# Performance work log

Measured on AMD Instinct MI355X. Metric: run time of the kernel, lower is better.

Reference implementation:

```python
import jax, jax.numpy as jnp
import numpy as np

AGENT_RADIUS = 0.3
B, F, H1, H21, H22, C, K = 262144, 5, 128, 32, 32, 2, 8


def _linear_init(k, fan_in, fan_out):
    lim = 1.0 / np.sqrt(fan_in)
    kw, kb = jax.random.split(k)
    W = jax.random.uniform(kw, (fan_out, fan_in), jnp.float32, -lim, lim)
    b = jax.random.uniform(kb, (fan_out,), jnp.float32, -lim, lim)
    return W, b


def setup_inputs() -> dict:
    key = jax.random.key(0)
    ks = jax.random.split(key, 9)
    W1, b1 = _linear_init(ks[0], F, H1)
    W21, b21 = _linear_init(ks[1], H1, H21)
    W22, b22 = _linear_init(ks[2], H1, H22)
    W31, b31 = _linear_init(ks[3], H21, C)
    W32, b32 = _linear_init(ks[4], H22, C)
    x = jax.random.normal(ks[5], (B, F), jnp.float32)
    mean = jax.random.normal(ks[6], (F,), jnp.float32) * 0.1
    std = jax.random.uniform(ks[7], (F,), jnp.float32, 0.5, 1.5)
    obs_xy = jax.random.uniform(ks[8], (K, 2), jnp.float32, -10.0, 10.0)
    obstacles = jnp.concatenate([obs_xy, jnp.full((K, 1), 0.5, jnp.float32)], axis=1)  # [K,3] = (ox,oy,r)
    return {"x": x, "mean": mean, "std": std,
            "W1": W1, "b1": b1, "W21": W21, "b21": b21, "W22": W22, "b22": b22,
            "W31": W31, "b31": b31, "W32": W32, "b32": b32,
            "obstacles": obstacles, "sgn": 1}


def _barriernet(x, mean, std, W1, b1, W21, b21, W22, b22, W31, b31, W32, b32, obstacles):
    nB = x.shape[0]
    x0 = x * std + mean
    h1 = jax.nn.relu(x @ W1.T + b1)                 # [B, H1]
    x21 = jax.nn.relu(h1 @ W21.T + b21)             # [B, H21]
    x22 = jax.nn.relu(h1 @ W22.T + b22)             # [B, H22]
    x31 = x21 @ W31.T + b31                          # [B, 2]  QP linear term p
    x32 = 4.0 * jax.nn.sigmoid(x22 @ W32.T + b32)    # [B, 2]  CBF class-K gains

    xo = x0 * std + mean  # module denormalizes twice inside dCBF (faithful to source)
    px, py, theta = xo[:, 0], xo[:, 1], xo[:, 2]
    oppx, oppy = xo[:, 3], xo[:, 4]
    cos_t, sin_t = jnp.cos(theta), jnp.sin(theta)

    # K static obstacles (broadcast) + 1 per-sample opponent -> nobs = K+1
    ox = jnp.concatenate([jnp.broadcast_to(obstacles[:, 0], (nB, K)), oppx[:, None]], axis=1)
    oy = jnp.concatenate([jnp.broadcast_to(obstacles[:, 1], (nB, K)), oppy[:, None]], axis=1)
    orr = jnp.concatenate([jnp.broadcast_to(obstacles[:, 2], (nB, K)),
                           jnp.full((nB, 1), AGENT_RADIUS, x.dtype)], axis=1)
    dx = px[:, None] - ox                            # [B, nobs]
    dy = py[:, None] - oy
    barrier = dx * dx + dy * dy - orr * orr          # [B, nobs]
    LgLf1 = 2.0 * dx * cos_t[:, None] + 2.0 * dy * sin_t[:, None]

    # QP: min 0.5 u^T I u + p^T u  s.t.  g1*u1 <= h  (second G column is 0)
    g1 = -LgLf1                                      # [B, nobs]
    hvec = (x32[:, 0] * x32[:, 1])[:, None] * barrier
    safe_g = jnp.where(g1 != 0.0, g1, 1.0)
    ratio = hvec / safe_g
    upper = jnp.min(jnp.where(g1 > 0.0, ratio, jnp.inf), axis=1)   # tightest u1 upper bound
    lower = jnp.max(jnp.where(g1 < 0.0, ratio, -jnp.inf), axis=1)  # tightest u1 lower bound
    u1 = jnp.clip(-x31[:, 0], lower, upper)          # exact KKT solution of the 1-D QP
    u2 = -x31[:, 1]                                  # unconstrained coordinate
    return jnp.stack([u1, u2], axis=1)               # [B, 2]


def reference(x, mean, std, W1, b1, W21, b21, W22, b22, W31, b31, W32, b32, obstacles, sgn):
    return _barriernet(x, mean, std, W1, b1, W21, b21, W22, b22, W31, b31, W32, b32, obstacles)
```

## Files before the change

### kernel.cpp

```cpp
#include <hip/hip_runtime.h>
#include <math.h>

typedef __attribute__((ext_vector_type(8))) short short8v;
typedef __attribute__((ext_vector_type(4))) float f32x4;

#define BLOCK 256
#define WPB   4
#define GRID  1024

__device__ inline unsigned int pk_bf16(float lo, float hi) {
    unsigned int r;
    asm("v_cvt_pk_bf16_f32 %0, %1, %2" : "=v"(r) : "v"(lo), "v"(hi));
    return r;
}
__device__ inline short8v as_s8(uint4 v) { union { uint4 u; short8v s; } c; c.u = v; return c.s; }

__global__ __launch_bounds__(BLOCK, 2) void bnet(
    const float* __restrict__ x,
    const float* __restrict__ meanp, const float* __restrict__ stdp,
    const float* __restrict__ W1,  const float* __restrict__ b1,
    const float* __restrict__ W21, const float* __restrict__ b21,
    const float* __restrict__ W22, const float* __restrict__ b22,
    const float* __restrict__ W31, const float* __restrict__ b31,
    const float* __restrict__ W32, const float* __restrict__ b32,
    const float* __restrict__ obstacles,
    float* __restrict__ out, int nB)
{
    __shared__ uint4 w1frag[8 * 64];
    __shared__ uint4 fragB[16 * 64];
    __shared__ float obl[32];

    const int t = threadIdx.x;

    {
        uint4 z = {0u, 0u, 0u, 0u};
        w1frag[t] = z; w1frag[t + 256] = z;
    }
    __syncthreads();
    if (t < 128) {
        int m = t & 15, g = t >> 4;
        int u = 16 * g + m;
        const float* wr = W1 + u * 5;
        uint4 v;
        v.x = pk_bf16(wr[0], wr[1]);
        v.y = pk_bf16(wr[2], wr[3]);
        v.z = pk_bf16(wr[4], b1[u]);
        v.w = 0u;
        w1frag[g * 64 + m] = v;
    }
    if (t < 8) {
        obl[t]      = obstacles[t * 3];
        obl[8 + t]  = obstacles[t * 3 + 1];
        float rr    = obstacles[t * 3 + 2];
        obl[16 + t] = rr * rr;
    }
    {
        const float4* w21v = (const float4*)W21;
        const float4* w22v = (const float4*)W22;
        #pragma unroll
        for (int e = 0; e < 4; ++e) {
            int g4   = t + e * 256;
            int uo   = g4 >> 5;
            int h0   = (g4 & 31) << 2;
            int ks   = h0 >> 5;
            int jh   = (h0 >> 4) & 1;
            int qq   = (h0 >> 2) & 3;
            int ln   = (qq << 4) | (uo & 15);
            int half = uo >> 4;
            float4 f1 = w21v[g4];
            float4 f2 = w22v[g4];
            unsigned int* dA = (unsigned int*)&fragB[(half * 4 + ks) * 64 + ln];
            unsigned int* dB = (unsigned int*)&fragB[(8 + half * 4 + ks) * 64 + ln];
            dA[jh * 2] = pk_bf16(f1.x, f1.y); dA[jh * 2 + 1] = pk_bf16(f1.z, f1.w);
            dB[jh * 2] = pk_bf16(f2.x, f2.y); dB[jh * 2 + 1] = pk_bf16(f2.z, f2.w);
        }
    }
    __syncthreads();

    const int lane = t & 63;
    const int q    = lane >> 4;
    const int r15  = lane & 15;
    const bool q0  = (q == 0);
    const int wid    = blockIdx.x * WPB + (t >> 6);
    const int nwaves = GRID * WPB;

    short8v bfr[16];
    #pragma unroll
    for (int i = 0; i < 16; ++i) bfr[i] = as_s8(fragB[i * 64 + lane]);

    float bi21[8], bi22[8];
    float c31_0[8], c31_1[8], c32_0[8], c32_1[8];
    {
        const int o = 4 * q;
        *(float4*)&bi21[0]  = *(const float4*)(b21 + o);
        *(float4*)&bi21[4]  = *(const float4*)(b21 + 16 + o);
        *(float4*)&bi22[0]  = *(const float4*)(b22 + o);
        *(float4*)&bi22[4]  = *(const float4*)(b22 + 16 + o);
        *(float4*)&c31_0[0] = *(const float4*)(W31 + o);
        *(float4*)&c31_0[4] = *(const float4*)(W31 + 16 + o);
        *(float4*)&c31_1[0] = *(const float4*)(W31 + 32 + o);
        *(float4*)&c31_1[4] = *(const float4*)(W31 + 48 + o);
        *(float4*)&c32_0[0] = *(const float4*)(W32 + o);
        *(float4*)&c32_0[4] = *(const float4*)(W32 + 16 + o);
        *(float4*)&c32_1[0] = *(const float4*)(W32 + 32 + o);
        *(float4*)&c32_1[4] = *(const float4*)(W32 + 48 + o);
    }
    const float b31_0 = b31[0], b31_1 = b31[1];
    const float b32_0 = b32[0], b32_1 = b32[1];

    float s2[5], ms[5];
    #pragma unroll
    for (int c = 0; c < 5; ++c) { float m = meanp[c], s = stdp[c]; s2[c] = s * s; ms[c] = fmaf(m, s, m); }

    const int ntiles = (nB + 15) >> 4;
    const int npairs = (ntiles + 1) >> 1;

    int pair = wid;
    if (pair >= npairs) return;

    float xrA[5], xrB[5];
    {
        int rA = pair * 32 + r15;      if (rA >= nB) rA = nB - 1;
        int rB = pair * 32 + 16 + r15; if (rB >= nB) rB = nB - 1;
        const float* pA = x + (size_t)rA * 5;
        const float* pB = x + (size_t)rB * 5;
        #pragma unroll
        for (int c = 0; c < 5; ++c) { xrA[c] = pA[c]; xrB[c] = pB[c]; }
    }

    while (true) {
        const int nxt = pair + nwaves;
        const bool has = nxt < npairs;
        float xA2[5], xB2[5];
        if (has) {
            int rA = nxt * 32 + r15;      if (rA >= nB) rA = nB - 1;
            int rB = nxt * 32 + 16 + r15; if (rB >= nB) rB = nB - 1;
            const float* pA = x + (size_t)rA * 5;
            const float* pB = x + (size_t)rB * 5;
            #pragma unroll
            for (int c = 0; c < 5; ++c) { xA2[c] = pA[c]; xB2[c] = pB[c]; }
        }
        const int baseA = pair * 32;

        short8v xfA, xfB;
        {
            float one = q0 ? 1.0f : 0.0f;
            uint4 va, vb;
            va.x = pk_bf16(q0 ? xrA[0] : 0.f, q0 ? xrA[1] : 0.f);
            va.y = pk_bf16(q0 ? xrA[2] : 0.f, q0 ? xrA[3] : 0.f);
            va.z = pk_bf16(q0 ? xrA[4] : 0.f, one);
            va.w = 0u;
            vb.x = pk_bf16(q0 ? xrB[0] : 0.f, q0 ? xrB[1] : 0.f);
            vb.y = pk_bf16(q0 ? xrB[2] : 0.f, q0 ? xrB[3] : 0.f);
            vb.z = pk_bf16(q0 ? xrB[4] : 0.f, one);
            vb.w = 0u;
            xfA = as_s8(va); xfB = as_s8(vb);
        }

        short8v afA[4], afB[4];
        #pragma unroll
        for (int ks = 0; ks < 4; ++ks) {
            f32x4 z = {0.f, 0.f, 0.f, 0.f};
            short8v w0 = as_s8(w1frag[(2 * ks) * 64 + lane]);
            short8v w1v = as_s8(w1frag[(2 * ks + 1) * 64 + lane]);
            f32x4 hA0 = __builtin_amdgcn_mfma_f32_16x16x32_bf16(w0,  xfA, z, 0, 0, 0);
            f32x4 hA1 = __builtin_amdgcn_mfma_f32_16x16x32_bf16(w1v, xfA, z, 0, 0, 0);
            f32x4 hB0 = __builtin_amdgcn_mfma_f32_16x16x32_bf16(w0,  xfB, z, 0, 0, 0);
            f32x4 hB1 = __builtin_amdgcn_mfma_f32_16x16x32_bf16(w1v, xfB, z, 0, 0, 0);
            uint4 va, vb;
            va.x = pk_bf16(fmaxf(hA0[0], 0.f), fmaxf(hA0[1], 0.f));
            va.y = pk_bf16(fmaxf(hA0[2], 0.f), fmaxf(hA0[3], 0.f));
            va.z = pk_bf16(fmaxf(hA1[0], 0.f), fmaxf(hA1[1], 0.f));
            va.w = pk_bf16(fmaxf(hA1[2], 0.f), fmaxf(hA1[3], 0.f));
            vb.x = pk_bf16(fmaxf(hB0[0], 0.f), fmaxf(hB0[1], 0.f));
            vb.y = pk_bf16(fmaxf(hB0[2], 0.f), fmaxf(hB0[3], 0.f));
            vb.z = pk_bf16(fmaxf(hB1[0], 0.f), fmaxf(hB1[1], 0.f));
            vb.w = pk_bf16(fmaxf(hB1[2], 0.f), fmaxf(hB1[3], 0.f));
            afA[ks] = as_s8(va); afB[ks] = as_s8(vb);
        }

        f32x4 a21aA = {bi21[0], bi21[1], bi21[2], bi21[3]};
        f32x4 a21bA = {bi21[4], bi21[5], bi21[6], bi21[7]};
        f32x4 a22aA = {bi22[0], bi22[1], bi22[2], bi22[3]};
        f32x4 a22bA = {bi22[4], bi22[5], bi22[6], bi22[7]};
        f32x4 a21aB = a21aA, a21bB = a21bA, a22aB = a22aA, a22bB = a22bA;
        #pragma unroll
        for (int ks = 0; ks < 4; ++ks) {
            a21aA = __builtin_amdgcn_mfma_f32_16x16x32_bf16(bfr[     ks], afA[ks], a21aA, 0, 0, 0);
            a21aB = __builtin_amdgcn_mfma_f32_16x16x32_bf16(bfr[     ks], afB[ks], a21aB, 0, 0, 0);
            a21bA = __builtin_amdgcn_mfma_f32_16x16x32_bf16(bfr[ 4 + ks], afA[ks], a21bA, 0, 0, 0);
            a21bB = __builtin_amdgcn_mfma_f32_16x16x32_bf16(bfr[ 4 + ks], afB[ks], a21bB, 0, 0, 0);
            a22aA = __builtin_amdgcn_mfma_f32_16x16x32_bf16(bfr[ 8 + ks], afA[ks], a22aA, 0, 0, 0);
            a22aB = __builtin_amdgcn_mfma_f32_16x16x32_bf16(bfr[ 8 + ks], afB[ks], a22aB, 0, 0, 0);
            a22bA = __builtin_amdgcn_mfma_f32_16x16x32_bf16(bfr[12 + ks], afA[ks], a22bA, 0, 0, 0);
            a22bB = __builtin_amdgcn_mfma_f32_16x16x32_bf16(bfr[12 + ks], afB[ks], a22bB, 0, 0, 0);
        }

        float p0A = 0.f, p1A = 0.f, p2A = 0.f, p3A = 0.f;
        float p0B = 0.f, p1B = 0.f, p2B = 0.f, p3B = 0.f;
        #pragma unroll
        for (int r = 0; r < 4; ++r) {
            float vA21a = fmaxf(a21aA[r], 0.f), vA21b = fmaxf(a21bA[r], 0.f);
            float vA22a = fmaxf(a22aA[r], 0.f), vA22b = fmaxf(a22bA[r], 0.f);
            float vB21a = fmaxf(a21aB[r], 0.f), vB21b = fmaxf(a21bB[r], 0.f);
            float vB22a = fmaxf(a22aB[r], 0.f), vB22b = fmaxf(a22bB[r], 0.f);
            p0A = fmaf(vA21a, c31_0[r], fmaf(vA21b, c31_0[4 + r], p0A));
            p1A = fmaf(vA21a, c31_1[r], fmaf(vA21b, c31_1[4 + r], p1A));
            p2A = fmaf(vA22a, c32_0[r], fmaf(vA22b, c32_0[4 + r], p2A));
            p3A = fmaf(vA22a, c32_1[r], fmaf(vA22b, c32_1[4 + r], p3A));
            p0B = fmaf(vB21a, c31_0[r], fmaf(vB21b, c31_0[4 + r], p0B));
            p1B = fmaf(vB21a, c31_1[r], fmaf(vB21b, c31_1[4 + r], p1B));
            p2B = fmaf(vB22a, c32_0[r], fmaf(vB22b, c32_0[4 + r], p2B));
            p3B = fmaf(vB22a, c32_1[r], fmaf(vB22b, c32_1[4 + r], p3B));
        }
        p0A += __shfl_xor(p0A, 16); p0A += __shfl_xor(p0A, 32);
        p1A += __shfl_xor(p1A, 16); p1A += __shfl_xor(p1A, 32);
        p2A += __shfl_xor(p2A, 16); p2A += __shfl_xor(p2A, 32);
        p3A += __shfl_xor(p3A, 16); p3A += __shfl_xor(p3A, 32);
        p0B += __shfl_xor(p0B, 16); p0B += __shfl_xor(p0B, 32);
        p1B += __shfl_xor(p1B, 16); p1B += __shfl_xor(p1B, 32);
        p2B += __shfl_xor(p2B, 16); p2B += __shfl_xor(p2B, 32);
        p3B += __shfl_xor(p3B, 16); p3B += __shfl_xor(p3B, 32);

        if (lane < 32) {
            const bool sa = (lane < 16);
            float x31_0 = (sa ? p0A : p0B) + b31_0;
            float x31_1 = (sa ? p1A : p1B) + b31_1;
            float t32_0 = (sa ? p2A : p2B) + b32_0;
            float t32_1 = (sa ? p3A : p3B) + b32_1;

            float s0v = __fdividef(4.f, 1.f + __expf(-t32_0));
            float s1v = __fdividef(4.f, 1.f + __expf(-t32_1));
            float hcoef = s0v * s1v;

            float xo[5];
            #pragma unroll
            for (int c = 0; c < 5; ++c) {
                float xc = sa ? xrA[c] : xrB[c];
                xo[c] = fmaf(xc, s2[c], ms[c]);
            }
            float px = xo[0], py = xo[1], th = xo[2], oppx = xo[3], oppy = xo[4];
            float st, ct;
            __sincosf(th, &st, &ct);

            float upper = INFINITY, lower = -INFINITY;
            #pragma unroll
            for (int j = 0; j < 9; ++j) {
                float ox  = (j < 8) ? obl[j]      : oppx;
                float oy  = (j < 8) ? obl[8 + j]  : oppy;
                float rr2 = (j < 8) ? obl[16 + j] : (0.3f * 0.3f);
                float dx = px - ox, dy = py - oy;
                float bar = fmaf(dx, dx, fmaf(dy, dy, -rr2));
                float g1  = -2.f * fmaf(dx, ct, dy * st);
                float ratio = __fdividef(hcoef * bar, (g1 != 0.f) ? g1 : 1.f);
                if (g1 > 0.f) upper = fminf(upper, ratio);
                if (g1 < 0.f) lower = fmaxf(lower, ratio);
            }
            float u1 = fminf(fmaxf(-x31_0, lower), upper);
            float u2 = -x31_1;

            int row = baseA + lane;
            if (row < nB) {
                float2 o; o.x = u1; o.y = u2;
                *reinterpret_cast<float2*>(out + 2 * (size_t)row) = o;
            }
        }

        if (!has) break;
        pair = nxt;
        #pragma unroll
        for (int c = 0; c < 5; ++c) { xrA[c] = xA2[c]; xrB[c] = xB2[c]; }
    }
}

extern "C" void kernel_launch(void* const* d_in, const int* in_sizes, int n_in,
                              void* d_out, int out_size, void* d_ws, size_t ws_size,
                              hipStream_t stream) {
    const float* x         = (const float*)d_in[0];
    const float* meanp     = (const float*)d_in[1];
    const float* stdp      = (const float*)d_in[2];
    const float* W1        = (const float*)d_in[3];
    const float* b1        = (const float*)d_in[4];
    const float* W21       = (const float*)d_in[5];
    const float* b21       = (const float*)d_in[6];
    const float* W22       = (const float*)d_in[7];
    const float* b22       = (const float*)d_in[8];
    const float* W31       = (const float*)d_in[9];
    const float* b31       = (const float*)d_in[10];
    const float* W32       = (const float*)d_in[11];
    const float* b32       = (const float*)d_in[12];
    const float* obstacles = (const float*)d_in[13];
    float* out = (float*)d_out;

    int nB = in_sizes[0] / 5;
    bnet<<<GRID, BLOCK, 0, stream>>>(
        x, meanp, stdp, W1, b1, W21, b21, W22, b22,
        W31, b31, W32, b32, obstacles, out, nB);
}
```

Before: 21.83 us.

## Replace persistent grid-stride loop with one-pair-per-wave grid and higher occupancy

Drops the persistent 1024-block loop with software prefetch. Instead it launches one wave per 32-row pair (2048 blocks for this size) and raises launch bounds to 4 blocks per CU. Layer-2 weight fragments and the bias/W3 coefficients are now read from LDS inside the compute path instead of being held in registers. The x loads are issued before the weight-staging prologue so their latency overlaps it. The aim is lower register pressure and more waves in flight to hide memory latency. The cost is that every block repeats the weight conversion into LDS, and obstacles, mean and std are read from global memory per wave.

```diff
diff --git a/kernel.cpp b/kernel.cpp
--- a/kernel.cpp
+++ b/kernel.cpp
@@ -5,8 +5,6 @@
 typedef __attribute__((ext_vector_type(4))) float f32x4;
 
 #define BLOCK 256
-#define WPB   4
-#define GRID  1024
 
 __device__ inline unsigned int pk_bf16(float lo, float hi) {
     unsigned int r;
@@ -14,8 +12,9 @@
     return r;
 }
 __device__ inline short8v as_s8(uint4 v) { union { uint4 u; short8v s; } c; c.u = v; return c.s; }
-
-__global__ __launch_bounds__(BLOCK, 2) void bnet(
+__device__ inline f32x4 as_f4(float4 v) { union { float4 u; f32x4 s; } c; c.u = v; return c.s; }
+
+__global__ __launch_bounds__(BLOCK, 4) void bnet(
     const float* __restrict__ x,
     const float* __restrict__ meanp, const float* __restrict__ stdp,
     const float* __restrict__ W1,  const float* __restrict__ b1,
@@ -28,9 +27,30 @@
 {
     __shared__ uint4 w1frag[8 * 64];
     __shared__ uint4 fragB[16 * 64];
-    __shared__ float obl[32];
-
-    const int t = threadIdx.x;
+    __shared__ float b2s[64];
+    __shared__ float w31s[64];
+    __shared__ float w32s[64];
+
+    const int t    = threadIdx.x;
+    const int lane = t & 63;
+    const int q    = lane >> 4;
+    const int r15  = lane & 15;
+    const bool q0  = (q == 0);
+
+    const int pair   = blockIdx.x * 4 + (t >> 6);
+    const int npairs = (nB + 31) >> 5;
+    const bool valid = pair < npairs;
+
+    float xrA[5], xrB[5];
+    {
+        int p  = valid ? pair : 0;
+        int rA = p * 32 + r15;      if (rA >= nB) rA = nB - 1;
+        int rB = p * 32 + 16 + r15; if (rB >= nB) rB = nB - 1;
+        const float* pA = x + (size_t)rA * 5;
+        const float* pB = x + (size_t)rB * 5;
+        #pragma unroll
+        for (int c = 0; c < 5; ++c) { xrA[c] = pA[c]; xrB[c] = pB[c]; }
+    }
 
     {
         uint4 z = {0u, 0u, 0u, 0u};
@@ -48,12 +68,9 @@
         v.w = 0u;
         w1frag[g * 64 + m] = v;
     }
-    if (t < 8) {
-        obl[t]      = obstacles[t * 3];
-        obl[8 + t]  = obstacles[t * 3 + 1];
-        float rr    = obstacles[t * 3 + 2];
-        obl[16 + t] = rr * rr;
-    }
+    if (t < 64)              b2s[t]        = (t < 32) ? b21[t] : b22[t - 32];
+    if (t >= 64 && t < 128)  w31s[t - 64]  = W31[t - 64];
+    if (t >= 128 && t < 192) w32s[t - 128] = W32[t - 128];
     {
         const float4* w21v = (const float4*)W21;
         const float4* w22v = (const float4*)W22;
@@ -76,200 +93,150 @@
         }
     }
     __syncthreads();
-
-    const int lane = t & 63;
-    const int q    = lane >> 4;
-    const int r15  = lane & 15;
-    const bool q0  = (q == 0);
-    const int wid    = blockIdx.x * WPB + (t >> 6);
-    const int nwaves = GRID * WPB;
-
-    short8v bfr[16];
-    #pragma unroll
-    for (int i = 0; i < 16; ++i) bfr[i] = as_s8(fragB[i * 64 + lane]);
-
-    float bi21[8], bi22[8];
-    float c31_0[8], c31_1[8], c32_0[8], c32_1[8];
-    {
-        const int o = 4 * q;
-        *(float4*)&bi21[0]  = *(const float4*)(b21 + o);
-        *(float4*)&bi21[4]  = *(const float4*)(b21 + 16 + o);
-        *(float4*)&bi22[0]  = *(const float4*)(b22 + o);
-        *(float4*)&bi22[4]  = *(const float4*)(b22 + 16 + o);
-        *(float4*)&c31_0[0] = *(const float4*)(W31 + o);
-        *(float4*)&c31_0[4] = *(const float4*)(W31 + 16 + o);
-        *(float4*)&c31_1[0] = *(const float4*)(W31 + 32 + o);
-        *(float4*)&c31_1[4] = *(const float4*)(W31 + 48 + o);
-        *(float4*)&c32_0[0] = *(const float4*)(W32 + o);
-        *(float4*)&c32_0[4] = *(const float4*)(W32 + 16 + o);
-        *(float4*)&c32_1[0] = *(const float4*)(W32 + 32 + o);
-        *(float4*)&c32_1[4] = *(const float4*)(W32 + 48 + o);
-    }
-    const float b31_0 = b31[0], b31_1 = b31[1];
-    const float b32_0 = b32[0], b32_1 = b32[1];
-
-    float s2[5], ms[5];
-    #pragma unroll
-    for (int c = 0; c < 5; ++c) { float m = meanp[c], s = stdp[c]; s2[c] = s * s; ms[c] = fmaf(m, s, m); }
-
-    const int ntiles = (nB + 15) >> 4;
-    const int npairs = (ntiles + 1) >> 1;
-
-    int pair = wid;
-    if (pair >= npairs) return;
-
-    float xrA[5], xrB[5];
-    {
-        int rA = pair * 32 + r15;      if (rA >= nB) rA = nB - 1;
-        int rB = pair * 32 + 16 + r15; if (rB >= nB) rB = nB - 1;
-        const float* pA = x + (size_t)rA * 5;
-        const float* pB = x + (size_t)rB * 5;
-        #pragma unroll
-        for (int c = 0; c < 5; ++c) { xrA[c] = pA[c]; xrB[c] = pB[c]; }
-    }
-
-    while (true) {
-        const int nxt = pair + nwaves;
-        const bool has = nxt < npairs;
-        float xA2[5], xB2[5];
-        if (has) {
-            int rA = nxt * 32 + r15;      if (rA >= nB) rA = nB - 1;
-            int rB = nxt * 32 + 16 + r15; if (rB >= nB) rB = nB - 1;
-            const float* pA = x + (size_t)rA * 5;
-            const float* pB = x + (size_t)rB * 5;
-            #pragma unroll
-            for (int c = 0; c < 5; ++c) { xA2[c] = pA[c]; xB2[c] = pB[c]; }
-        }
-        const int baseA = pair * 32;
-
-        short8v xfA, xfB;
-        {
-            float one = q0 ? 1.0f : 0.0f;
-            uint4 va, vb;
-            va.x = pk_bf16(q0 ? xrA[0] : 0.f, q0 ? xrA[1] : 0.f);
-            va.y = pk_bf16(q0 ? xrA[2] : 0.f, q0 ? xrA[3] : 0.f);
-            va.z = pk_bf16(q0 ? xrA[4] : 0.f, one);
-            va.w = 0u;
-            vb.x = pk_bf16(q0 ? xrB[0] : 0.f, q0 ? xrB[1] : 0.f);
-            vb.y = pk_bf16(q0 ? xrB[2] : 0.f, q0 ? xrB[3] : 0.f);
-            vb.z = pk_bf16(q0 ? xrB[4] : 0.f, one);
-            vb.w = 0u;
-            xfA = as_s8(va); xfB = as_s8(vb);
-        }
-
-        short8v afA[4], afB[4];
-        #pragma unroll
-        for (int ks = 0; ks < 4; ++ks) {
-            f32x4 z = {0.f, 0.f, 0.f, 0.f};
-            short8v w0 = as_s8(w1frag[(2 * ks) * 64 + lane]);
-            short8v w1v = as_s8(w1frag[(2 * ks + 1) * 64 + lane]);
-            f32x4 hA0 = __builtin_amdgcn_mfma_f32_16x16x32_bf16(w0,  xfA, z, 0, 0, 0);
-            f32x4 hA1 = __builtin_amdgcn_mfma_f32_16x16x32_bf16(w1v, xfA, z, 0, 0, 0);
-            f32x4 hB0 = __builtin_amdgcn_mfma_f32_16x16x32_bf16(w0,  xfB, z, 0, 0, 0);
-            f32x4 hB1 = __builtin_amdgcn_mfma_f32_16x16x32_bf16(w1v, xfB, z, 0, 0, 0);
-            uint4 va, vb;
-            va.x = pk_bf16(fmaxf(hA0[0], 0.f), fmaxf(hA0[1], 0.f));
-            va.y = pk_bf16(fmaxf(hA0[2], 0.f), fmaxf(hA0[3], 0.f));
-            va.z = pk_bf16(fmaxf(hA1[0], 0.f), fmaxf(hA1[1], 0.f));
-            va.w = pk_bf16(fmaxf(hA1[2], 0.f), fmaxf(hA1[3], 0.f));
-            vb.x = pk_bf16(fmaxf(hB0[0], 0.f), fmaxf(hB0[1], 0.f));
-            vb.y = pk_bf16(fmaxf(hB0[2], 0.f), fmaxf(hB0[3], 0.f));
-            vb.z = pk_bf16(fmaxf(hB1[0], 0.f), fmaxf(hB1[1], 0.f));
-            vb.w = pk_bf16(fmaxf(hB1[2], 0.f), fmaxf(hB1[3], 0.f));
-            afA[ks] = as_s8(va); afB[ks] = as_s8(vb);
-        }
-
-        f32x4 a21aA = {bi21[0], bi21[1], bi21[2], bi21[3]};
-        f32x4 a21bA = {bi21[4], bi21[5], bi21[6], bi21[7]};
-        f32x4 a22aA = {bi22[0], bi22[1], bi22[2], bi22[3]};
-        f32x4 a22bA = {bi22[4], bi22[5], bi22[6], bi22[7]};
-        f32x4 a21aB = a21aA, a21bB = a21bA, a22aB = a22aA, a22bB = a22bA;
-        #pragma unroll
-        for (int ks = 0; ks < 4; ++ks) {
-            a21aA = __builtin_amdgcn_mfma_f32_16x16x32_bf16(bfr[     ks], afA[ks], a21aA, 0, 0, 0);
-            a21aB = __builtin_amdgcn_mfma_f32_16x16x32_bf16(bfr[     ks], afB[ks], a21aB, 0, 0, 0);
-            a21bA = __builtin_amdgcn_mfma_f32_16x16x32_bf16(bfr[ 4 + ks], afA[ks], a21bA, 0, 0, 0);
-            a21bB = __builtin_amdgcn_mfma_f32_16x16x32_bf16(bfr[ 4 + ks], afB[ks], a21bB, 0, 0, 0);
-            a22aA = __builtin_amdgcn_mfma_f32_16x16x32_bf16(bfr[ 8 + ks], afA[ks], a22aA, 0, 0, 0);
-            a22aB = __builtin_amdgcn_mfma_f32_16x16x32_bf16(bfr[ 8 + ks], afB[ks], a22aB, 0, 0, 0);
-            a22bA = __builtin_amdgcn_mfma_f32_16x16x32_bf16(bfr[12 + ks], afA[ks], a22bA, 0, 0, 0);
-            a22bB = __builtin_amdgcn_mfma_f32_16x16x32_bf16(bfr[12 + ks], afB[ks], a22bB, 0, 0, 0);
-        }
-
-        float p0A = 0.f, p1A = 0.f, p2A = 0.f, p3A = 0.f;
-        float p0B = 0.f, p1B = 0.f, p2B = 0.f, p3B = 0.f;
-        #pragma unroll
-        for (int r = 0; r < 4; ++r) {
-            float vA21a = fmaxf(a21aA[r], 0.f), vA21b = fmaxf(a21bA[r], 0.f);
-            float vA22a = fmaxf(a22aA[r], 0.f), vA22b = fmaxf(a22bA[r], 0.f);
-            float vB21a = fmaxf(a21aB[r], 0.f), vB21b = fmaxf(a21bB[r], 0.f);
-            float vB22a = fmaxf(a22aB[r], 0.f), vB22b = fmaxf(a22bB[r], 0.f);
-            p0A = fmaf(vA21a, c31_0[r], fmaf(vA21b, c31_0[4 + r], p0A));
-            p1A = fmaf(vA21a, c31_1[r], fmaf(vA21b, c31_1[4 + r], p1A));
-            p2A = fmaf(vA22a, c32_0[r], fmaf(vA22b, c32_0[4 + r], p2A));
-            p3A = fmaf(vA22a, c32_1[r], fmaf(vA22b, c32_1[4 + r], p3A));
-            p0B = fmaf(vB21a, c31_0[r], fmaf(vB21b, c31_0[4 + r], p0B));
-            p1B = fmaf(vB21a, c31_1[r], fmaf(vB21b, c31_1[4 + r], p1B));
-            p2B = fmaf(vB22a, c32_0[r], fmaf(vB22b, c32_0[4 + r], p2B));
-            p3B = fmaf(vB22a, c32_1[r], fmaf(vB22b, c32_1[4 + r], p3B));
-        }
-        p0A += __shfl_xor(p0A, 16); p0A += __shfl_xor(p0A, 32);
-        p1A += __shfl_xor(p1A, 16); p1A += __shfl_xor(p1A, 32);
-        p2A += __shfl_xor(p2A, 16); p2A += __shfl_xor(p2A, 32);
-        p3A += __shfl_xor(p3A, 16); p3A += __shfl_xor(p3A, 32);
-        p0B += __shfl_xor(p0B, 16); p0B += __shfl_xor(p0B, 32);
-        p1B += __shfl_xor(p1B, 16); p1B += __shfl_xor(p1B, 32);
-        p2B += __shfl_xor(p2B, 16); p2B += __shfl_xor(p2B, 32);
-        p3B += __shfl_xor(p3B, 16); p3B += __shfl_xor(p3B, 32);
-
-        if (lane < 32) {
-            const bool sa = (lane < 16);
-            float x31_0 = (sa ? p0A : p0B) + b31_0;
-            float x31_1 = (sa ? p1A : p1B) + b31_1;
-            float t32_0 = (sa ? p2A : p2B) + b32_0;
-            float t32_1 = (sa ? p3A : p3B) + b32_1;
-
-            float s0v = __fdividef(4.f, 1.f + __expf(-t32_0));
-            float s1v = __fdividef(4.f, 1.f + __expf(-t32_1));
-            float hcoef = s0v * s1v;
-
-            float xo[5];
-            #pragma unroll
-            for (int c = 0; c < 5; ++c) {
-                float xc = sa ? xrA[c] : xrB[c];
-                xo[c] = fmaf(xc, s2[c], ms[c]);
+    if (!valid) return;
+
+    const int baseA = pair * 32;
+
+    short8v xfA, xfB;
+    {
+        float one = q0 ? 1.0f : 0.0f;
+        uint4 va, vb;
+        va.x = pk_bf16(q0 ? xrA[0] : 0.f, q0 ? xrA[1] : 0.f);
+        va.y = pk_bf16(q0 ? xrA[2] : 0.f, q0 ? xrA[3] : 0.f);
+        va.z = pk_bf16(q0 ? xrA[4] : 0.f, one);
+        va.w = 0u;
+        vb.x = pk_bf16(q0 ? xrB[0] : 0.f, q0 ? xrB[1] : 0.f);
+        vb.y = pk_bf16(q0 ? xrB[2] : 0.f, q0 ? xrB[3] : 0.f);
+        vb.z = pk_bf16(q0 ? xrB[4] : 0.f, one);
+        vb.w = 0u;
+        xfA = as_s8(va); xfB = as_s8(vb);
+    }
+
+    short8v afA[4], afB[4];
+    #pragma unroll
+    for (int ks = 0; ks < 4; ++ks) {
+        f32x4 z = {0.f, 0.f, 0.f, 0.f};
+        short8v w0  = as_s8(w1frag[(2 * ks) * 64 + lane]);
+        short8v w1v = as_s8(w1frag[(2 * ks + 1) * 64 + lane]);
+        f32x4 hA0 = __builtin_amdgcn_mfma_f32_16x16x32_bf16(w0,  xfA, z, 0, 0, 0);
+        f32x4 hA1 = __builtin_amdgcn_mfma_f32_16x16x32_bf16(w1v, xfA, z, 0, 0, 0);
+        f32x4 hB0 = __builtin_amdgcn_mfma_f32_16x16x32_bf16(w0,  xfB, z, 0, 0, 0);
+        f32x4 hB1 = __builtin_amdgcn_mfma_f32_16x16x32_bf16(w1v, xfB, z, 0, 0, 0);
+        uint4 va, vb;
+        va.x = pk_bf16(fmaxf(hA0[0], 0.f), fmaxf(hA0[1], 0.f));
+        va.y = pk_bf16(fmaxf(hA0[2], 0.f), fmaxf(hA0[3], 0.f));
+        va.z = pk_bf16(fmaxf(hA1[0], 0.f), fmaxf(hA1[1], 0.f));
+        va.w = pk_bf16(fmaxf(hA1[2], 0.f), fmaxf(hA1[3], 0.f));
+        vb.x = pk_bf16(fmaxf(hB0[0], 0.f), fmaxf(hB0[1], 0.f));
+        vb.y = pk_bf16(fmaxf(hB0[2], 0.f), fmaxf(hB0[3], 0.f));
+        vb.z = pk_bf16(fmaxf(hB1[0], 0.f), fmaxf(hB1[1], 0.f));
+        vb.w = pk_bf16(fmaxf(hB1[2], 0.f), fmaxf(hB1[3], 0.f));
+        afA[ks] = as_s8(va); afB[ks] = as_s8(vb);
+    }
+
+    const float4* b2v = (const float4*)b2s;
+    f32x4 a21aA = as_f4(b2v[q]);
+    f32x4 a21bA = as_f4(b2v[4 + q]);
+    f32x4 a22aA = as_f4(b2v[8 + q]);
+    f32x4 a22bA = as_f4(b2v[12 + q]);
+    f32x4 a21aB = a21aA, a21bB = a21bA, a22aB = a22aA, a22bB = a22bA;
+    #pragma unroll
+    for (int ks = 0; ks < 4; ++ks) {
+        short8v f21a = as_s8(fragB[(     ks) * 64 + lane]);
+        short8v f21b = as_s8(fragB[( 4 + ks) * 64 + lane]);
+        short8v f22a = as_s8(fragB[( 8 + ks) * 64 + lane]);
+        short8v f22b = as_s8(fragB[(12 + ks) * 64 + lane]);
+        a21aA = __builtin_amdgcn_mfma_f32_16x16x32_bf16(f21a, afA[ks], a21aA, 0, 0, 0);
+        a21aB = __builtin_amdgcn_mfma_f32_16x16x32_bf16(f21a, afB[ks], a21aB, 0, 0, 0);
+        a21bA = __builtin_amdgcn_mfma_f32_16x16x32_bf16(f21b, afA[ks], a21bA, 0, 0, 0);
+        a21bB = __builtin_amdgcn_mfma_f32_16x16x32_bf16(f21b, afB[ks], a21bB, 0, 0, 0);
+        a22aA = __builtin_amdgcn_mfma_f32_16x16x32_bf16(f22a, afA[ks], a22aA, 0, 0, 0);
+        a22aB = __builtin_amdgcn_mfma_f32_16x16x32_bf16(f22a, afB[ks], a22aB, 0, 0, 0);
+        a22bA = __builtin_amdgcn_mfma_f32_16x16x32_bf16(f22b, afA[ks], a22bA, 0, 0, 0);
+        a22bB = __builtin_amdgcn_mfma_f32_16x16x32_bf16(f22b, afB[ks], a22bB, 0, 0, 0);
+    }
+
+    float vA21[8], vA22[8], vB21[8], vB22[8];
+    #pragma unroll
+    for (int r = 0; r < 4; ++r) {
+        vA21[r] = fmaxf(a21aA[r], 0.f); vA21[4 + r] = fmaxf(a21bA[r], 0.f);
+        vA22[r] = fmaxf(a22aA[r], 0.f); vA22[4 + r] = fmaxf(a22bA[r], 0.f);
+        vB21[r] = fmaxf(a21aB[r], 0.f); vB21[4 + r] = fmaxf(a21bB[r], 0.f);
+        vB22[r] = fmaxf(a22aB[r], 0.f); vB22[4 + r] = fmaxf(a22bB[r], 0.f);
+    }
+    float pA[4], pB[4];
+    #pragma unroll
+    for (int hsel = 0; hsel < 4; ++hsel) {
+        const float* cof = (hsel < 2) ? w31s : w32s;
+        const float* vavA = (hsel < 2) ? vA21 : vA22;
+        const float* vavB = (hsel < 2) ? vB21 : vB22;
+        int off = (hsel & 1) * 32;
+        float4 clo = *(const float4*)(cof + off + 4 * q);
+        float4 chi = *(const float4*)(cof + off + 16 + 4 * q);
+        float sA = 0.f, sB = 0.f;
+        sA = fmaf(vavA[0], clo.x, sA); sA = fmaf(vavA[1], clo.y, sA);
+        sA = fmaf(vavA[2], clo.z, sA); sA = fmaf(vavA[3], clo.w, sA);
+        sA = fmaf(vavA[4], chi.x, sA); sA = fmaf(vavA[5], chi.y, sA);
+        sA = fmaf(vavA[6], chi.z, sA); sA = fmaf(vavA[7], chi.w, sA);
+        sB = fmaf(vavB[0], clo.x, sB); sB = fmaf(vavB[1], clo.y, sB);
+        sB = fmaf(vavB[2], clo.z, sB); sB = fmaf(vavB[3], clo.w, sB);
+        sB = fmaf(vavB[4], chi.x, sB); sB = fmaf(vavB[5], chi.y, sB);
+        sB = fmaf(vavB[6], chi.z, sB); sB = fmaf(vavB[7], chi.w, sB);
+        sA += __shfl_xor(sA, 16); sA += __shfl_xor(sA, 32);
+        sB += __shfl_xor(sB, 16); sB += __shfl_xor(sB, 32);
+        pA[hsel] = sA; pB[hsel] = sB;
+    }
+
+    if (lane < 32) {
+        const bool sa = (lane < 16);
+        float x31_0 = (sa ? pA[0] : pB[0]) + b31[0];
+        float x31_1 = (sa ? pA[1] : pB[1]) + b31[1];
+        float t32_0 = (sa ? pA[2] : pB[2]) + b32[0];
+        float t32_1 = (sa ? pA[3] : pB[3]) + b32[1];
+
+        float s0v = __fdividef(4.f, 1.f + __expf(-t32_0));
+        float s1v = __fdividef(4.f, 1.f + __expf(-t32_1));
+        float hcoef = s0v * s1v;
+
+        float xo[5];
+        #pragma unroll
+        for (int c = 0; c < 5; ++c) {
+            float m = meanp[c], s = stdp[c];
+            float xc = sa ? xrA[c] : xrB[c];
+            float x0 = fmaf(xc, s, m);
+            xo[c] = fmaf(x0, s, m);
+        }
+        float px = xo[0], py = xo[1], th = xo[2], oppx = xo[3], oppy = xo[4];
+        float st, ct;
+        __sincosf(th, &st, &ct);
+
+        float upper = INFINITY, lower = -INFINITY;
+        #pragma unroll
+        for (int j = 0; j < 9; ++j) {
+            float ox, oy, rr2;
+            if (j < 8) {
+                ox = obstacles[j * 3];
+                oy = obstacles[j * 3 + 1];
+                float rr = obstacles[j * 3 + 2];
+                rr2 = rr * rr;
+            } else {
+                ox = oppx; oy = oppy; rr2 = 0.3f * 0.3f;
             }
-            float px = xo[0], py = xo[1], th = xo[2], oppx = xo[3], oppy = xo[4];
-            float st, ct;
-            __sincosf(th, &st, &ct);
-
-            float upper = INFINITY, lower = -INFINITY;
-            #pragma unroll
-            for (int j = 0; j < 9; ++j) {
-                float ox  = (j < 8) ? obl[j]      : oppx;
-                float oy  = (j < 8) ? obl[8 + j]  : oppy;
-                float rr2 = (j < 8) ? obl[16 + j] : (0.3f * 0.3f);
-                float dx = px - ox, dy = py - oy;
-                float bar = fmaf(dx, dx, fmaf(dy, dy, -rr2));
-                float g1  = -2.f * fmaf(dx, ct, dy * st);
-                float ratio = __fdividef(hcoef * bar, (g1 != 0.f) ? g1 : 1.f);
-                if (g1 > 0.f) upper = fminf(upper, ratio);
-                if (g1 < 0.f) lower = fmaxf(lower, ratio);
-            }
-            float u1 = fminf(fmaxf(-x31_0, lower), upper);
-            float u2 = -x31_1;
-
-            int row = baseA + lane;
-            if (row < nB) {
-                float2 o; o.x = u1; o.y = u2;
-                *reinterpret_cast<float2*>(out + 2 * (size_t)row) = o;
-            }
-        }
-
-        if (!has) break;
-        pair = nxt;
-        #pragma unroll
-        for (int c = 0; c < 5; ++c) { xrA[c] = xA2[c]; xrB[c] = xB2[c]; }
+            float dx = px - ox, dy = py - oy;
+            float bar = fmaf(dx, dx, fmaf(dy, dy, -rr2));
+            float g1  = -2.f * fmaf(dx, ct, dy * st);
+            float ratio = __fdividef(hcoef * bar, (g1 != 0.f) ? g1 : 1.f);
+            if (g1 > 0.f) upper = fminf(upper, ratio);
+            if (g1 < 0.f) lower = fmaxf(lower, ratio);
+        }
+        float u1 = fminf(fmaxf(-x31_0, lower), upper);
+        float u2 = -x31_1;
+
+        int row = baseA + lane;
+        if (row < nB) {
+            float2 o; o.x = u1; o.y = u2;
+            *reinterpret_cast<float2*>(out + 2 * (size_t)row) = o;
+        }
     }
 }
 
@@ -293,7 +260,9 @@
     float* out = (float*)d_out;
 
     int nB = in_sizes[0] / 5;
-    bnet<<<GRID, BLOCK, 0, stream>>>(
+    int npairs = (nB + 31) / 32;
+    int grid = (npairs + 3) / 4;
+    bnet<<<grid, BLOCK, 0, stream>>>(
         x, meanp, stdp, W1, b1, W21, b21, W22, b22,
         W31, b31, W32, b32, obstacles, out, nB);
 }
```

Measured after the change: 23.88 us. 1.09x slower.
